# Performance work log

Measured on AMD Instinct MI355X. Metric: run time of the kernel, lower is better.

The kernel has to match this reference:

```python
import jax, jax.numpy as jnp
import numpy as np

B, S, D, N = 8, 4096, 768, 64


def setup_inputs() -> dict:
    key = jax.random.key(0)
    k1, k2 = jax.random.split(key)
    word_vectors = jax.random.normal(k1, (B, S, D), dtype=jnp.float32)
    sent_rep_token_ids = jnp.sort(jax.random.randint(k2, (B, N), 0, S), axis=1)
    sent_rep_mask = jnp.ones((B, N), dtype=jnp.float32)
    # sent_lengths: each row must sum exactly to S (torch.split contract).
    rng = np.random.default_rng(0)
    lens = np.stack([
        np.diff(np.concatenate([[0], np.sort(rng.choice(np.arange(1, S), N - 1, replace=False)), [S]]))
        for _ in range(B)
    ])
    sent_lengths = jnp.asarray(lens, dtype=jnp.int64) if jax.config.jax_enable_x64 else jnp.asarray(lens, dtype=jnp.int32)
    sent_lengths_mask = jnp.ones((B, N), dtype=jnp.float32)
    return {
        "word_vectors": word_vectors,
        "sent_rep_token_ids": sent_rep_token_ids,
        "sent_rep_mask": sent_rep_mask,
        "sent_lengths": sent_lengths,
        "sent_lengths_mask": sent_lengths_mask,
    }


def reference(word_vectors, sent_rep_token_ids, sent_rep_mask, sent_lengths, sent_lengths_mask):
    b, s, d = word_vectors.shape
    n = sent_lengths.shape[1]
    dt = word_vectors.dtype

    # --- sent_rep_tokens branch: gather CLS-style token per sentence ---
    rep_vec = jnp.take_along_axis(word_vectors, sent_rep_token_ids[:, :, None], axis=1)  # [B,N,D]
    rep_vec = rep_vec * sent_rep_mask[:, :, None].astype(dt)

    # --- mean_tokens branch: ragged per-segment mean via segment_sum ---
    ends = jnp.cumsum(sent_lengths, axis=1)                      # [B,N] exclusive-end offsets
    pos = jnp.arange(s)
    seg = jax.vmap(lambda e: jnp.searchsorted(e, pos, side='right'))(ends)  # [B,S] segment id per token
    gseg = (seg + jnp.arange(b)[:, None] * n).reshape(-1)        # global segment ids [B*S]
    flat = word_vectors.reshape(b * s, d)
    sums = jax.ops.segment_sum(flat, gseg, num_segments=b * n).reshape(b, n, d)
    counts = jax.ops.segment_sum((flat != 0).astype(dt), gseg, num_segments=b * n).reshape(b, n, d)
    mean = sums / jnp.maximum(counts, 1)
    # fallback to word_vectors[0,0] when a segment has zero nonzero entries (original semantics)
    all_zero = (counts.sum(axis=-1) == 0)                        # [B,N]
    mean = jnp.where(all_zero[:, :, None], word_vectors[0, 0], mean)
    mean_vec = mean * sent_lengths_mask[:, :, None].astype(dt)

    out_vectors = jnp.concatenate([rep_vec, mean_vec], axis=1)   # [B,2N,D]
    out_masks = jnp.concatenate([sent_rep_mask, sent_lengths_mask], axis=1)  # [B,2N]
    return out_vectors, out_masks
```

## Files before the change

### kernel.cpp

```cpp
#include <hip/hip_runtime.h>

#define BB 8
#define SS 4096
#define DD 768
#define NN 64
#define D4 (DD / 4)
#define CHT 128
#define MAXCH 96
#define NREC (BB * MAXCH)

__global__ __launch_bounds__(256) void chunk_kernel(
    const float* __restrict__ wv,
    const int* __restrict__ lens,
    float* __restrict__ ws_sum,
    unsigned char* __restrict__ ws_cnt)
{
    const int cidx = blockIdx.x;
    const int b    = blockIdx.y;
    const int g    = blockIdx.z;
    const int tid  = threadIdx.x;
    const int lane = tid & 63;
    const int w    = tid >> 6;

    const int l    = lens[b * NN + lane];
    const int nchl = (l + CHT - 1) >> 7;
    int inclen = l, inch = nchl;
    #pragma unroll
    for (int off = 1; off < 64; off <<= 1) {
        int a = __shfl_up(inclen, off); if (lane >= off) inclen += a;
        int c = __shfl_up(inch,   off); if (lane >= off) inch   += c;
    }
    const int total_ch = __shfl(inch, 63);
    if (cidx >= total_ch) return;

    unsigned long long m = __ballot(inch > cidx);
    const int n         = __ffsll(m) - 1;
    const int seg_len   = __shfl(l, n);
    const int seg_start = __shfl(inclen, n) - seg_len;
    const int ch_base   = __shfl(inch, n) - __shfl(nchl, n);
    const int t0 = seg_start + (cidx - ch_base) * CHT;
    const int t1 = min(seg_start + seg_len, t0 + CHT);

    const int col4 = g * 64 + lane;
    const float4* base = (const float4*)wv + (size_t)b * SS * D4 + col4;

    float4 s = make_float4(0.f, 0.f, 0.f, 0.f);
    float4 c = make_float4(0.f, 0.f, 0.f, 0.f);
    #pragma unroll 4
    for (int t = t0 + w; t < t1; t += 4) {
        float4 v = base[(size_t)t * D4];
        s.x += v.x; s.y += v.y; s.z += v.z; s.w += v.w;
        c.x += (v.x != 0.f) ? 1.f : 0.f;
        c.y += (v.y != 0.f) ? 1.f : 0.f;
        c.z += (v.z != 0.f) ? 1.f : 0.f;
        c.w += (v.w != 0.f) ? 1.f : 0.f;
    }

    __shared__ float4 s_s[4][64];
    __shared__ float4 s_c[4][64];
    s_s[w][lane] = s;
    s_c[w][lane] = c;
    __syncthreads();

    if (tid < 64) {
        float4 S = make_float4(0.f, 0.f, 0.f, 0.f);
        float4 C = make_float4(0.f, 0.f, 0.f, 0.f);
        #pragma unroll
        for (int j = 0; j < 4; ++j) {
            float4 a = s_s[j][tid], d = s_c[j][tid];
            S.x += a.x; S.y += a.y; S.z += a.z; S.w += a.w;
            C.x += d.x; C.y += d.y; C.z += d.z; C.w += d.w;
        }
        const size_t rec = (size_t)(b * MAXCH + cidx);
        ((float4*)ws_sum)[rec * D4 + g * 64 + tid] = S;
        uchar4 u;
        u.x = (unsigned char)C.x; u.y = (unsigned char)C.y;
        u.z = (unsigned char)C.z; u.w = (unsigned char)C.w;
        ((uchar4*)ws_cnt)[rec * D4 + g * 64 + tid] = u;
    }
}

__global__ __launch_bounds__(256) void finalize_kernel(
    const float* __restrict__ wv,
    const int* __restrict__ rep_ids,
    const float* __restrict__ rep_mask,
    const int* __restrict__ lens,
    const float* __restrict__ len_mask,
    const float* __restrict__ ws_sum,
    const unsigned char* __restrict__ ws_cnt,
    float* __restrict__ out)
{
    __shared__ float s_part[4];
    __shared__ int s_info[2];
    const int sgid = blockIdx.x;
    const int b = sgid >> 6, n = sgid & 63;
    const int tid = threadIdx.x;
    const int lane = tid & 63;

    if (tid < 64) {
        const int l    = lens[b * NN + tid];
        const int nchl = (l + CHT - 1) >> 7;
        int inch = nchl;
        #pragma unroll
        for (int off = 1; off < 64; off <<= 1) {
            int a = __shfl_up(inch, off); if (lane >= off) inch += a;
        }
        if (tid == n) { s_info[0] = inch - nchl; s_info[1] = nchl; }
    }
    __syncthreads();
    const int ch_base = s_info[0];
    const int K       = s_info[1];
    const bool active = tid < D4;

    float4 S = make_float4(0,0,0,0), C = S;
    if (active) {
        for (int k = 0; k < K; ++k) {
            const size_t rec = (size_t)(b * MAXCH + ch_base + k);
            float4 sv = ((const float4*)ws_sum)[rec * D4 + tid];
            uchar4 cv = ((const uchar4*)ws_cnt)[rec * D4 + tid];
            S.x += sv.x; S.y += sv.y; S.z += sv.z; S.w += sv.w;
            C.x += (float)cv.x; C.y += (float)cv.y;
            C.z += (float)cv.z; C.w += (float)cv.w;
        }
    }

    float tot = C.x + C.y + C.z + C.w;
    #pragma unroll
    for (int off = 32; off; off >>= 1) tot += __shfl_xor(tot, off);
    if ((tid & 63) == 0) s_part[tid >> 6] = tot;
    __syncthreads();
    const float total = s_part[0] + s_part[1] + s_part[2] + s_part[3];

    if (active) {
        float4 mean;
        mean.x = S.x / fmaxf(C.x, 1.f);
        mean.y = S.y / fmaxf(C.y, 1.f);
        mean.z = S.z / fmaxf(C.z, 1.f);
        mean.w = S.w / fmaxf(C.w, 1.f);
        if (total == 0.f) mean = ((const float4*)wv)[tid];

        const float lm = len_mask[sgid];
        mean.x *= lm; mean.y *= lm; mean.z *= lm; mean.w *= lm;

        float4* out4 = (float4*)out;
        out4[(size_t)(b * 2 * NN + NN + n) * D4 + tid] = mean;

        const int   rid = rep_ids[sgid];
        const float rm  = rep_mask[sgid];
        float4 rv = ((const float4*)wv)[(size_t)(b * SS + rid) * D4 + tid];
        rv.x *= rm; rv.y *= rm; rv.z *= rm; rv.w *= rm;
        out4[(size_t)(b * 2 * NN + n) * D4 + tid] = rv;

        if (tid == 0) {
            float* masks = out + (size_t)BB * 2 * NN * DD;
            masks[b * 2 * NN + n]      = rm;
            masks[b * 2 * NN + NN + n] = lm;
        }
    }
}

extern "C" void kernel_launch(void* const* d_in, const int* in_sizes, int n_in,
                              void* d_out, int out_size, void* d_ws, size_t ws_size,
                              hipStream_t stream) {
    const float* wv       = (const float*)d_in[0];
    const int*   rep_ids  = (const int*)d_in[1];
    const float* rep_mask = (const float*)d_in[2];
    const int*   lens     = (const int*)d_in[3];
    const float* len_mask = (const float*)d_in[4];
    float*       out      = (float*)d_out;
    float*         ws_sum = (float*)d_ws;
    unsigned char* ws_cnt = (unsigned char*)d_ws + (size_t)NREC * DD * 4;

    dim3 gridB(MAXCH, BB, 3);
    chunk_kernel<<<gridB, 256, 0, stream>>>(wv, lens, ws_sum, ws_cnt);
    finalize_kernel<<<BB * NN, 256, 0, stream>>>(wv, rep_ids, rep_mask, lens,
                                                 len_mask, ws_sum, ws_cnt, out);
}
```

Before: 164.9 us.

## Stream token rows into LDS via async global_load_lds double buffering

The chunk kernel now uses one 192-thread block per chunk covering the full 768-wide row, instead of splitting columns across three blocks. Token rows are staged into a double-buffered LDS tile with global_load_lds DMA, and a manual vmcnt wait plus s_barrier overlaps the next tile's loads with accumulation of the current one. This drops the cross-wave shared-memory reduction, but it cuts the grid to a third of the blocks and adds a barrier for every 6 rows, so less parallelism may be available to hide memory latency.

```diff
diff --git a/kernel.cpp b/kernel.cpp
--- a/kernel.cpp
+++ b/kernel.cpp
@@ -1,4 +1,5 @@
 #include <hip/hip_runtime.h>
+#include <stdint.h>
 
 #define BB 8
 #define SS 4096
@@ -8,16 +9,26 @@
 #define CHT 128
 #define MAXCH 96
 #define NREC (BB * MAXCH)
-
-__global__ __launch_bounds__(256) void chunk_kernel(
+#define TROWS 6
+#define BLOCK 192
+
+__device__ __forceinline__ void dma16(const float* g, float4* l) {
+    __builtin_amdgcn_global_load_lds(
+        (const __attribute__((address_space(1))) unsigned int*)g,
+        (__attribute__((address_space(3))) unsigned int*)l,
+        16, 0, 0);
+}
+
+__global__ __launch_bounds__(BLOCK) void chunk_kernel(
     const float* __restrict__ wv,
     const int* __restrict__ lens,
     float* __restrict__ ws_sum,
     unsigned char* __restrict__ ws_cnt)
 {
+    __shared__ float4 tiles[2][TROWS][D4];
+
     const int cidx = blockIdx.x;
     const int b    = blockIdx.y;
-    const int g    = blockIdx.z;
     const int tid  = threadIdx.x;
     const int lane = tid & 63;
     const int w    = tid >> 6;
@@ -41,43 +52,55 @@
     const int t0 = seg_start + (cidx - ch_base) * CHT;
     const int t1 = min(seg_start + seg_len, t0 + CHT);
 
-    const int col4 = g * 64 + lane;
-    const float4* base = (const float4*)wv + (size_t)b * SS * D4 + col4;
+    const float* wvb = wv + (size_t)b * SS * DD;
+
+    auto stage = [&](int bf, int tb) {
+        #pragma unroll
+        for (int rr = 0; rr < 2; ++rr) {
+            const int r   = 2 * w + rr;
+            const int tok = min(tb + r, t1 - 1);
+            const float* g = wvb + (size_t)tok * DD + lane * 4;
+            float4* ld = &tiles[bf][r][lane];
+            dma16(g,       ld);
+            dma16(g + 256, ld + 64);
+            dma16(g + 512, ld + 128);
+        }
+    };
 
     float4 s = make_float4(0.f, 0.f, 0.f, 0.f);
     float4 c = make_float4(0.f, 0.f, 0.f, 0.f);
-    #pragma unroll 4
-    for (int t = t0 + w; t < t1; t += 4) {
-        float4 v = base[(size_t)t * D4];
-        s.x += v.x; s.y += v.y; s.z += v.z; s.w += v.w;
-        c.x += (v.x != 0.f) ? 1.f : 0.f;
-        c.y += (v.y != 0.f) ? 1.f : 0.f;
-        c.z += (v.z != 0.f) ? 1.f : 0.f;
-        c.w += (v.w != 0.f) ? 1.f : 0.f;
-    }
-
-    __shared__ float4 s_s[4][64];
-    __shared__ float4 s_c[4][64];
-    s_s[w][lane] = s;
-    s_c[w][lane] = c;
-    __syncthreads();
-
-    if (tid < 64) {
-        float4 S = make_float4(0.f, 0.f, 0.f, 0.f);
-        float4 C = make_float4(0.f, 0.f, 0.f, 0.f);
-        #pragma unroll
-        for (int j = 0; j < 4; ++j) {
-            float4 a = s_s[j][tid], d = s_c[j][tid];
-            S.x += a.x; S.y += a.y; S.z += a.z; S.w += a.w;
-            C.x += d.x; C.y += d.y; C.z += d.z; C.w += d.w;
-        }
-        const size_t rec = (size_t)(b * MAXCH + cidx);
-        ((float4*)ws_sum)[rec * D4 + g * 64 + tid] = S;
-        uchar4 u;
-        u.x = (unsigned char)C.x; u.y = (unsigned char)C.y;
-        u.z = (unsigned char)C.z; u.w = (unsigned char)C.w;
-        ((uchar4*)ws_cnt)[rec * D4 + g * 64 + tid] = u;
-    }
+    const int ntiles = (t1 - t0 + TROWS - 1) / TROWS;
+
+    stage(0, t0);
+    for (int it = 0; it < ntiles; ++it) {
+        const int bf = it & 1;
+        if (it + 1 < ntiles) {
+            stage(bf ^ 1, t0 + (it + 1) * TROWS);
+            __asm__ __volatile__("s_waitcnt vmcnt(6)" ::: "memory");
+        } else {
+            __asm__ __volatile__("s_waitcnt vmcnt(0)" ::: "memory");
+        }
+        __asm__ __volatile__("s_barrier" ::: "memory");
+
+        const int tb   = t0 + it * TROWS;
+        const int rmax = min(TROWS, t1 - tb);
+        for (int r = 0; r < rmax; ++r) {
+            float4 v = tiles[bf][r][tid];
+            s.x += v.x; s.y += v.y; s.z += v.z; s.w += v.w;
+            c.x += (v.x != 0.f) ? 1.f : 0.f;
+            c.y += (v.y != 0.f) ? 1.f : 0.f;
+            c.z += (v.z != 0.f) ? 1.f : 0.f;
+            c.w += (v.w != 0.f) ? 1.f : 0.f;
+        }
+        __asm__ __volatile__("s_barrier" ::: "memory");
+    }
+
+    const size_t rec = (size_t)(b * MAXCH + cidx);
+    ((float4*)ws_sum)[rec * D4 + tid] = s;
+    uchar4 u;
+    u.x = (unsigned char)c.x; u.y = (unsigned char)c.y;
+    u.z = (unsigned char)c.z; u.w = (unsigned char)c.w;
+    ((uchar4*)ws_cnt)[rec * D4 + tid] = u;
 }
 
 __global__ __launch_bounds__(256) void finalize_kernel(
@@ -171,8 +194,8 @@
     float*         ws_sum = (float*)d_ws;
     unsigned char* ws_cnt = (unsigned char*)d_ws + (size_t)NREC * DD * 4;
 
-    dim3 gridB(MAXCH, BB, 3);
-    chunk_kernel<<<gridB, 256, 0, stream>>>(wv, lens, ws_sum, ws_cnt);
+    dim3 gridB(MAXCH, BB);
+    chunk_kernel<<<gridB, BLOCK, 0, stream>>>(wv, lens, ws_sum, ws_cnt);
     finalize_kernel<<<BB * NN, 256, 0, stream>>>(wv, rep_ids, rep_mask, lens,
                                                  len_mask, ws_sum, ws_cnt, out);
 }
```

Result: no change. 167.6 us (+1.6%).
